# Kernel optimization log

Hardware: AMD Instinct MI355X
Metric: run time of the kernel (lower is better)

The kernel has to match this reference:

```python
import jax, jax.numpy as jnp
import numpy as np
import math

D_MODEL = 1024
NUM_HEADS = 16
D_K = D_MODEL // NUM_HEADS
SEQ = 2048
BATCH = 2


def setup_inputs() -> dict:
    key = jax.random.key(0)
    ks = jax.random.split(key, 11)
    s = 1.0 / math.sqrt(D_MODEL)
    return {
        "query": jax.random.normal(ks[0], (SEQ, BATCH, D_MODEL), jnp.float32),
        "key": jax.random.normal(ks[1], (SEQ, BATCH, D_MODEL), jnp.float32),
        "value": jax.random.normal(ks[2], (SEQ, BATCH, D_MODEL), jnp.float32),
        "Wq": jax.random.normal(ks[3], (D_MODEL, D_MODEL), jnp.float32) * s,
        "bq": jnp.zeros((D_MODEL,), jnp.float32),
        "Wk": jax.random.normal(ks[4], (D_MODEL, D_MODEL), jnp.float32) * s,
        "bk": jnp.zeros((D_MODEL,), jnp.float32),
        "Wv": jax.random.normal(ks[5], (D_MODEL, D_MODEL), jnp.float32) * s,
        "bv": jnp.zeros((D_MODEL,), jnp.float32),
        "Wo": jax.random.normal(ks[6], (D_MODEL, D_MODEL), jnp.float32) * s,
        "bo": jnp.zeros((D_MODEL,), jnp.float32),
    }


def _split_heads(x):
    # [S, B, D] -> [S, B, H, d_k]
    S, B, _ = x.shape
    return x.reshape(S, B, NUM_HEADS, D_K)


def reference(query, key, value, Wq, bq, Wk, bk, Wv, bv, Wo, bo):
    # torch Linear: y = x @ W.T + b
    q = _split_heads(query @ Wq.T + bq)   # [S,B,H,dk]
    k = _split_heads(key @ Wk.T + bk)
    v = _split_heads(value @ Wv.T + bv)
    # score[q,k,b,h] = sum_d q[q,b,h,d] k[k,b,h,d]
    score = jnp.einsum('qbhd,kbhd->qkbh', q, k) / math.sqrt(D_K)
    attn = jax.nn.softmax(score, axis=1)  # Softmax(dim=1) == over key axis
    out = jnp.einsum('qkbh,kbhd->qbhd', attn, v)  # [S,B,H,dk]
    S, B = out.shape[0], out.shape[1]
    out = out.reshape(S, B, NUM_HEADS * D_K)
    return out @ Wo.T + bo
```

## Files before the change

### kernel.cpp

```cpp
#include <hip/hip_runtime.h>

typedef unsigned short u16;
typedef short s16x8 __attribute__((ext_vector_type(8)));
typedef short s16x4 __attribute__((ext_vector_type(4)));
typedef float f32x4 __attribute__((ext_vector_type(4)));

#define MFMA_BF16(A,B,C) __builtin_amdgcn_mfma_f32_16x16x32_bf16(A,B,C,0,0,0)

#if defined(__has_builtin)
#if __has_builtin(__builtin_amdgcn_mfma_f32_16x16x16bf16_1k)
#define HAVE_MFMA16 1
#define MFMA16(A,B,C) __builtin_amdgcn_mfma_f32_16x16x16bf16_1k(A,B,C,0,0,0)
#endif
#endif

static constexpr int DMODEL = 1024;
static constexpr int SEQn   = 2048;
static constexpr int BATCH  = 2;
static constexpr int NH     = 16;
static constexpr int DKn    = 64;
static constexpr int ROWST  = BATCH*DMODEL;
static constexpr float QSCALE = 0.18033688011112042f;

__device__ __forceinline__ u16 f2bf(float f) {
    unsigned u = __builtin_bit_cast(unsigned, f);
    u += 0x7FFFu + ((u >> 16) & 1u);
    return (u16)(u >> 16);
}

#if defined(__has_builtin)
#if __has_builtin(__builtin_amdgcn_cvt_pk_bf16_f32)
#define HAVE_PKBF16 1
#endif
#endif
#ifdef HAVE_PKBF16
typedef __bf16 bf16x2 __attribute__((ext_vector_type(2)));
__device__ __forceinline__ unsigned pk2bf(float a, float b) {
    bf16x2 t = __builtin_amdgcn_cvt_pk_bf16_f32(a, b);
    return __builtin_bit_cast(unsigned, t);
}
#else
__device__ __forceinline__ unsigned pk2bf(float a, float b) {
    return (unsigned)f2bf(a) | ((unsigned)f2bf(b) << 16);
}
#endif

__device__ __forceinline__ void gld_lds16(const u16* g, u16* l) {
    __builtin_amdgcn_global_load_lds(
        (const __attribute__((address_space(1))) void*)g,
        (__attribute__((address_space(3))) void*)l,
        16, 0, 0);
}

__global__ void cvt_bf16(const float* __restrict__ q, const float* __restrict__ k,
                         const float* __restrict__ v, const float* __restrict__ wq,
                         const float* __restrict__ wk, const float* __restrict__ wv,
                         const float* __restrict__ wo,
                         u16* __restrict__ qb, u16* __restrict__ kb, u16* __restrict__ vb,
                         u16* __restrict__ wqb, u16* __restrict__ wkb, u16* __restrict__ wvb,
                         u16* __restrict__ wob)
{
    const int z = blockIdx.z;
    const float* S; u16* D; size_t n;
    switch (z) {
        case 0: S = q;  D = qb;  n = 4194304; break;
        case 1: S = k;  D = kb;  n = 4194304; break;
        case 2: S = v;  D = vb;  n = 4194304; break;
        case 3: S = wq; D = wqb; n = 1048576; break;
        case 4: S = wk; D = wkb; n = 1048576; break;
        case 5: S = wv; D = wvb; n = 1048576; break;
        default: S = wo; D = wob; n = 1048576; break;
    }
    const size_t i = ((size_t)blockIdx.x * 256 + threadIdx.x) * 8;
    if (i >= n) return;
    float4 a = *(const float4*)(S + i);
    float4 b = *(const float4*)(S + i + 4);
    uint4 pk;
    pk.x = pk2bf(a.x, a.y); pk.y = pk2bf(a.z, a.w);
    pk.z = pk2bf(b.x, b.y); pk.w = pk2bf(b.z, b.w);
    *(uint4*)(D + i) = pk;
}

__global__ __launch_bounds__(512, 2)
void gemm_qkv(const u16* __restrict__ A0, const u16* __restrict__ A1, const u16* __restrict__ A2,
              const u16* __restrict__ W0, const u16* __restrict__ W1, const u16* __restrict__ W2,
              const float* __restrict__ B0, const float* __restrict__ B1, const float* __restrict__ B2,
              void* __restrict__ O0, void* __restrict__ O1, void* __restrict__ O2)
{
    const u16* A; const u16* W; const float* bias; void* Outv;
    const int z = blockIdx.z;
    if (z == 0)      { A = A0; W = W0; bias = B0; Outv = O0; }
    else if (z == 1) { A = A1; W = W1; bias = B1; Outv = O1; }
    else             { A = A2; W = W2; bias = B2; Outv = O2; }

    __shared__ alignas(16) u16 SH[65536];

    const int tid  = threadIdx.x;
    const int wave = tid >> 6, lane = tid & 63;
    const int quad = lane >> 4, col = lane & 15;
    const int wr = wave >> 2;
    const int wn = wave & 3;
    const int m0 = blockIdx.y * 256, n0 = blockIdx.x * 256;

    f32x4 acc[8][4];
#pragma unroll
    for (int i = 0; i < 8; ++i)
#pragma unroll
        for (int j = 0; j < 4; ++j) acc[i][j] = f32x4{0.f,0.f,0.f,0.f};

    auto stageT = [&](int t) {
        const int slot = t & 3;
        const int k0 = t * 32;
        u16* Ad = SH + slot * 8192;
        u16* Bd = SH + 32768 + slot * 8192;
#pragma unroll
        for (int i = 0; i < 2; ++i) {
            const int idx = i*512 + wave*64 + lane;
            const int row = idx >> 2;
            const int s = idx & 3;
            const int g = s ^ ((row >> 1) & 3);
            gld_lds16(A + (size_t)(m0 + row)*DMODEL + k0 + g*8, Ad + (i*512 + wave*64)*8);
            gld_lds16(W + (size_t)(n0 + row)*DMODEL + k0 + g*8, Bd + (i*512 + wave*64)*8);
        }
    };

    auto compute = [&](int slot) {
        const u16* As_ = SH + slot * 8192;
        const u16* Bs_ = SH + 32768 + slot * 8192;
        s16x8 bfr[4], af[4];
#pragma unroll
        for (int fj = 0; fj < 4; ++fj) {
            const int rb = wn*64 + fj*16 + col;
            bfr[fj] = *(const s16x8*)&Bs_[rb*32 + (quad ^ ((rb >> 1) & 3))*8];
        }
#pragma unroll
        for (int fi = 0; fi < 4; ++fi) {
            const int ra = wr*128 + fi*16 + col;
            af[fi] = *(const s16x8*)&As_[ra*32 + (quad ^ ((ra >> 1) & 3))*8];
        }
        __builtin_amdgcn_s_setprio(1);
#pragma unroll
        for (int fi = 0; fi < 4; ++fi)
#pragma unroll
            for (int fj = 0; fj < 4; ++fj)
                acc[fi][fj] = MFMA_BF16(af[fi], bfr[fj], acc[fi][fj]);
        __builtin_amdgcn_s_setprio(0);
#pragma unroll
        for (int fi = 0; fi < 4; ++fi) {
            const int ra = wr*128 + (4 + fi)*16 + col;
            af[fi] = *(const s16x8*)&As_[ra*32 + (quad ^ ((ra >> 1) & 3))*8];
        }
        __builtin_amdgcn_s_setprio(1);
#pragma unroll
        for (int fi = 0; fi < 4; ++fi)
#pragma unroll
            for (int fj = 0; fj < 4; ++fj)
                acc[4 + fi][fj] = MFMA_BF16(af[fi], bfr[fj], acc[4 + fi][fj]);
        __builtin_amdgcn_s_setprio(0);
    };

    stageT(0); stageT(1); stageT(2);

    for (int t = 0; t < 30; ++t) {
        asm volatile("s_waitcnt vmcnt(8)" ::: "memory");
        __builtin_amdgcn_s_barrier();
        asm volatile("" ::: "memory");
        if (t < 29) stageT(t + 3);
        compute(t & 3);
    }
    asm volatile("s_waitcnt vmcnt(4)" ::: "memory");
    __builtin_amdgcn_s_barrier();
    asm volatile("" ::: "memory");
    compute(2);
    asm volatile("s_waitcnt vmcnt(0)" ::: "memory");
    __builtin_amdgcn_s_barrier();
    asm volatile("" ::: "memory");
    compute(3);

    float bv[4];
#pragma unroll
    for (int fj = 0; fj < 4; ++fj) bv[fj] = bias[n0 + wn*64 + fj*16 + col];

    if (z < 2) {
        u16* Out = (u16*)Outv;
        const float osc = (z == 0) ? QSCALE : 1.f;
#pragma unroll
        for (int fi = 0; fi < 8; ++fi)
#pragma unroll
            for (int fj = 0; fj < 4; ++fj) {
                const int n = n0 + wn*64 + fj*16 + col;
#pragma unroll
                for (int r = 0; r < 4; ++r) {
                    const int m = m0 + wr*128 + fi*16 + quad*4 + r;
                    Out[(size_t)m*DMODEL + n] = f2bf((acc[fi][fj][r] + bv[fj])*osc);
                }
            }
    } else {
        u16* Out = (u16*)Outv;
        u16* T = SH;
#pragma unroll
        for (int p = 0; p < 2; ++p) {
            __syncthreads();
            if (wr == p) {
#pragma unroll
                for (int fi = 0; fi < 8; ++fi)
#pragma unroll
                    for (int fj = 0; fj < 4; ++fj) {
                        const int nl = wn*64 + fj*16 + col;
#pragma unroll
                        for (int r = 0; r < 4; ++r)
                            T[(fi*16 + quad*4 + r)*257 + nl] = f2bf(acc[fi][fj][r] + bv[fj]);
                    }
            }
            __syncthreads();
            const int s0 = (m0 >> 1) + p*64;
#pragma unroll
            for (int t = 0; t < 8; ++t) {
                const int c = t*512 + tid;
                const int sc = c & 7;
                const int nl = (c >> 3) & 255;
                const int bb = c >> 11;
                u16 e[8];
#pragma unroll
                for (int j = 0; j < 8; ++j)
                    e[j] = T[((sc*8 + j)*2 + bb)*257 + nl];
                uint4 x; __builtin_memcpy(&x, e, 16);
                const int ng = n0 + nl, hh = ng >> 6, dd = ng & 63;
                *(uint4*)(Out + (((size_t)bb*NH + hh)*DKn + dd)*SEQn + s0 + sc*8) = x;
            }
        }
    }
}

template<bool FINAL>
__global__ __launch_bounds__(256, 2)
void gemm_bt(const u16* __restrict__ A0, const u16* __restrict__ A1, const u16* __restrict__ A2,
             const u16* __restrict__ W0, const u16* __restrict__ W1, const u16* __restrict__ W2,
             const float* __restrict__ B0, const float* __restrict__ B1, const float* __restrict__ B2,
             void* __restrict__ O0, void* __restrict__ O1, void* __restrict__ O2)
{
    const u16* A; const u16* W; const float* bias; void* Outv;
    const int z = blockIdx.z;
    if (z == 0)      { A = A0; W = W0; bias = B0; Outv = O0; }
    else if (z == 1) { A = A1; W = W1; bias = B1; Outv = O1; }
    else             { A = A2; W = W2; bias = B2; Outv = O2; }

    __shared__ alignas(16) u16 SH[FINAL ? 128*128 : 129*128];
    u16* As = SH;
    u16* Bs = SH + 128*64;

    const int tid  = threadIdx.x;
    const int wave = tid >> 6, lane = tid & 63;
    const int quad = lane >> 4, col = lane & 15;
    const int wm = wave & 1, wn = wave >> 1;
    const int m0 = blockIdx.y * 128, n0 = blockIdx.x * 128;

    f32x4 acc[4][4];
#pragma unroll
    for (int i = 0; i < 4; ++i)
#pragma unroll
        for (int j = 0; j < 4; ++j) acc[i][j] = f32x4{0.f,0.f,0.f,0.f};

    for (int kt = 0; kt < DMODEL/64; ++kt) {
        if (kt) __syncthreads();
        const int k0 = kt*64;
#pragma unroll
        for (int i = 0; i < 4; ++i) {
            const int chunk = (i*4 + wave)*64 + lane;
            const int row = chunk >> 3;
            const int kk = ((chunk & 7) ^ (row & 7)) * 8;
            gld_lds16(A + (size_t)(m0 + row)*DMODEL + (k0 + kk), &As[(i*4 + wave)*512]);
            gld_lds16(W + (size_t)(n0 + row)*DMODEL + (k0 + kk), &Bs[(i*4 + wave)*512]);
        }
        __syncthreads();
#pragma unroll
        for (int ks = 0; ks < 2; ++ks) {
            s16x8 af[4], bfr[4];
#pragma unroll
            for (int t = 0; t < 4; ++t) {
                const int ra = wm*64 + t*16 + col;
                af[t]  = *(const s16x8*)&As[ra*64 + (((ks*4 + quad) ^ (ra & 7))*8)];
                const int rb = wn*64 + t*16 + col;
                bfr[t] = *(const s16x8*)&Bs[rb*64 + (((ks*4 + quad) ^ (rb & 7))*8)];
            }
#pragma unroll
            for (int i = 0; i < 4; ++i)
#pragma unroll
                for (int j = 0; j < 4; ++j)
                    acc[i][j] = MFMA_BF16(af[i], bfr[j], acc[i][j]);
        }
    }

    float bv[4];
#pragma unroll
    for (int j = 0; j < 4; ++j) bv[j] = bias[n0 + wn*64 + j*16 + col];

    if (FINAL) {
#pragma unroll
        for (int i = 0; i < 4; ++i)
#pragma unroll
            for (int j = 0; j < 4; ++j) {
                const int n = n0 + wn*64 + j*16 + col;
#pragma unroll
                for (int r = 0; r < 4; ++r) {
                    const int m = m0 + wm*64 + i*16 + quad*4 + r;
                    ((float*)Outv)[(size_t)m*DMODEL + n] = acc[i][j][r] + bv[j];
                }
            }
    } else {
        const float osc = (z == 0) ? QSCALE : 1.f;
        const int SST = (z == 2) ? 129 : 128;
        __syncthreads();
#pragma unroll
        for (int i = 0; i < 4; ++i)
#pragma unroll
            for (int j = 0; j < 4; ++j) {
                const int nl = wn*64 + j*16 + col;
#pragma unroll
                for (int r = 0; r < 4; ++r) {
                    const int ml = wm*64 + i*16 + quad*4 + r;
                    SH[ml*SST + nl] = f2bf((acc[i][j][r] + bv[j])*osc);
                }
            }
        __syncthreads();
        u16* Out = (u16*)Outv;
        if (z < 2) {
#pragma unroll
            for (int t = 0; t < 8; ++t) {
                const int c = t*256 + tid;
                const int ml = c >> 4, n8 = (c & 15)*8;
                uint4 x = *(const uint4*)&SH[ml*128 + n8];
                *(uint4*)(Out + (size_t)(m0 + ml)*DMODEL + n0 + n8) = x;
            }
        } else {
            const int s0 = m0 >> 1;
#pragma unroll
            for (int t = 0; t < 8; ++t) {
                const int c = t*256 + tid;
                const int sc = c & 7;
                const int nl = (c >> 3) & 127;
                const int bb = c >> 10;
                u16 e[8];
#pragma unroll
                for (int j = 0; j < 8; ++j)
                    e[j] = SH[((sc*8 + j)*2 + bb)*129 + nl];
                uint4 x; __builtin_memcpy(&x, e, 16);
                const int ng = n0 + nl, hh = ng >> 6, dd = ng & 63;
                *(uint4*)(Out + (((size_t)bb*NH + hh)*DKn + dd)*SEQn + s0 + sc*8) = x;
            }
        }
    }
}

__global__ __launch_bounds__(256, 4)
void attn_fwd(const u16* __restrict__ Q, const u16* __restrict__ K,
              const u16* __restrict__ Vt, u16* __restrict__ O)
{
    __shared__ alignas(16) u16 Ks[128*64];
    __shared__ alignas(16) u16 Vs[64*128];

    const int qt = blockIdx.x, bh = blockIdx.y;
    const int b = bh >> 4, h = bh & 15;
    const int tid = threadIdx.x;
    const int wave = tid >> 6, lane = tid & 63;
    const int quad = lane >> 4, col = lane & 15;

    const u16* Qh = Q + b*DMODEL + h*DKn;
    const u16* Kh = K + b*DMODEL + h*DKn;
    const u16* Vh = Vt + (size_t)bh*DKn*SEQn;

    const int q0 = qt*64 + wave*16;
    s16x8 qf[2];
#pragma unroll
    for (int ks = 0; ks < 2; ++ks)
        qf[ks] = *(const s16x8*)(Qh + (size_t)(q0 + col)*ROWST + ks*32 + quad*8);

    const short ONEBF = (short)0x3F80;
    const s16x4 ones = {ONEBF, ONEBF, ONEBF, ONEBF};

    f32x4 o[4];
    f32x4 lacc = f32x4{0.f,0.f,0.f,0.f};
#pragma unroll
    for (int dt = 0; dt < 4; ++dt) o[dt] = f32x4{0.f,0.f,0.f,0.f};

    for (int kt = 0; kt < SEQn/128; ++kt) {
        __syncthreads();
#pragma unroll
        for (int i = 0; i < 4; ++i) {
            {
                const int chunk = (i*4 + wave)*64 + lane;
                const int row = chunk >> 3;
                const int kk = ((chunk & 7) ^ (row & 7))*8;
                gld_lds16(Kh + (size_t)(kt*128 + row)*ROWST + kk, &Ks[(i*4 + wave)*512]);
            }
            {
                const int chunk = (i*4 + wave)*64 + lane;
                const int d = chunk >> 4;
                const int kk = ((chunk & 15) ^ (d & 15))*8;
                gld_lds16(Vh + (size_t)d*SEQn + kt*128 + kk, &Vs[(i*4 + wave)*512]);
            }
        }
        __syncthreads();

        f32x4 sfr[8];
#pragma unroll
        for (int nt = 0; nt < 8; ++nt) sfr[nt] = f32x4{0.f,0.f,0.f,0.f};
#pragma unroll
        for (int ks = 0; ks < 2; ++ks) {
            s16x8 kf[8];
#pragma unroll
            for (int nt = 0; nt < 8; ++nt) {
                const int key = nt*16 + col;
                kf[nt] = *(const s16x8*)&Ks[key*64 + (((ks*4 + quad) ^ (key & 7))*8)];
            }
#pragma unroll
            for (int nt = 0; nt < 8; ++nt)
                sfr[nt] = MFMA_BF16(kf[nt], qf[ks], sfr[nt]);
        }

        s16x4 pk[8];
#pragma unroll
        for (int nt = 0; nt < 8; ++nt) {
            float p0 = __builtin_amdgcn_exp2f(sfr[nt][0]);
            float p1 = __builtin_amdgcn_exp2f(sfr[nt][1]);
            float p2 = __builtin_amdgcn_exp2f(sfr[nt][2]);
            float p3 = __builtin_amdgcn_exp2f(sfr[nt][3]);
            unsigned w[2] = { pk2bf(p0, p1), pk2bf(p2, p3) };
            __builtin_memcpy(&pk[nt], w, 8);
        }

#ifdef HAVE_MFMA16
#pragma unroll
        for (int c = 0; c < 8; ++c) {
            lacc = MFMA16(ones, pk[c], lacc);
#pragma unroll
            for (int dt = 0; dt < 4; ++dt) {
                const int d = dt*16 + col;
                const s16x4 vfr = *(const s16x4*)&Vs[d*128 + (((c*2 + (quad>>1)) ^ (d & 15))*8) + (quad & 1)*4];
                o[dt] = MFMA16(vfr, pk[c], o[dt]);
            }
        }
#else
        const int a0 = (32*(quad & 1) + col)*4;
        const s16x8 ones8 = {ONEBF,ONEBF,ONEBF,ONEBF,ONEBF,ONEBF,ONEBF,ONEBF};
#pragma unroll
        for (int ksp = 0; ksp < 4; ++ksp) {
            int pA[2], pB[2];
            __builtin_memcpy(pA, &pk[ksp*2], 8);
            __builtin_memcpy(pB, &pk[ksp*2 + 1], 8);
            int w[4];
#pragma unroll
            for (int hh = 0; hh < 2; ++hh) {
                const int ad = a0 + hh*64;
                const int xA0 = __builtin_amdgcn_ds_bpermute(ad, pA[0]);
                const int xA1 = __builtin_amdgcn_ds_bpermute(ad, pA[1]);
                const int xB0 = __builtin_amdgcn_ds_bpermute(ad, pB[0]);
                const int xB1 = __builtin_amdgcn_ds_bpermute(ad, pB[1]);
                w[hh*2]     = (quad >= 2) ? xB0 : xA0;
                w[hh*2 + 1] = (quad >= 2) ? xB1 : xA1;
            }
            s16x8 pfr; __builtin_memcpy(&pfr, w, 16);
            lacc = MFMA_BF16(ones8, pfr, lacc);
#pragma unroll
            for (int dt = 0; dt < 4; ++dt) {
                const int d = dt*16 + col;
                const s16x8 vfr = *(const s16x8*)&Vs[d*128 + (((ksp*4 + quad) ^ (d & 15))*8)];
                o[dt] = MFMA_BF16(vfr, pfr, o[dt]);
            }
        }
#endif
    }

    const float inv = 1.f / lacc[0];
    const int srow = q0 + col;
#pragma unroll
    for (int dt = 0; dt < 4; ++dt) {
        uint2 pko;
        pko.x = pk2bf(o[dt][0]*inv, o[dt][1]*inv);
        pko.y = pk2bf(o[dt][2]*inv, o[dt][3]*inv);
        *(uint2*)(O + ((size_t)srow*BATCH + b)*DMODEL + h*DKn + dt*16 + quad*4) = pko;
    }
}

extern "C" void kernel_launch(void* const* d_in, const int* in_sizes, int n_in,
                              void* d_out, int out_size, void* d_ws, size_t ws_size,
                              hipStream_t stream)
{
    const float* q  = (const float*)d_in[0];
    const float* k  = (const float*)d_in[1];
    const float* v  = (const float*)d_in[2];
    const float* Wq = (const float*)d_in[3];
    const float* bq = (const float*)d_in[4];
    const float* Wk = (const float*)d_in[5];
    const float* bk = (const float*)d_in[6];
    const float* Wv = (const float*)d_in[7];
    const float* bv = (const float*)d_in[8];
    const float* Wo = (const float*)d_in[9];
    const float* bo = (const float*)d_in[10];
    float* out = (float*)d_out;

    const size_t N = (size_t)SEQn * BATCH * DMODEL;
    const size_t NW = (size_t)DMODEL * DMODEL;
    u16* qb  = (u16*)d_ws;
    u16* kb  = qb + N;
    u16* vb  = kb + N;
    u16* wqb = vb + N;
    u16* wkb = wqb + NW;
    u16* wvb = wkb + NW;
    u16* wob = wvb + NW;
    u16* Qw  = wob + NW;
    u16* Kw  = Qw + N;
    u16* Vtw = Kw + N;
    u16* AO  = qb;

    cvt_bf16<<<dim3(2048, 1, 7), 256, 0, stream>>>(q, k, v, Wq, Wk, Wv, Wo,
                                                   qb, kb, vb, wqb, wkb, wvb, wob);
    gemm_qkv<<<dim3(4, 16, 3), 512, 0, stream>>>(qb, kb, vb, wqb, wkb, wvb,
                                                 bq, bk, bv, Qw, Kw, Vtw);
    attn_fwd<<<dim3(32, 32), 256, 0, stream>>>(Qw, Kw, Vtw, AO);
    gemm_bt<true><<<dim3(8, 32, 1), 256, 0, stream>>>(AO, AO, AO, wob, wob, wob,
                                                      bo, bo, bo, out, out, out);
}
```

Measured before the change: 229.5 us.

## Load K/V fragments directly from global memory with XCD-aware block mapping

The attention kernel drops its shared-memory staging of K and V tiles and the two barriers per iteration. Each wave now reads its MFMA fragments straight from global memory. Blocks are remapped on a 1-D grid so that every XCD handles four (batch, head) pairs, which keeps K/V reuse inside one L2. The softmax denominator moves from an extra MFMA against a ones vector to an fp32 running sum reduced with shuffles. The risk is that the four waves now re-read the same K/V data through cache with less coalesced accesses instead of sharing it in LDS.

```diff
diff --git a/kernel.cpp b/kernel.cpp
--- a/kernel.cpp
+++ b/kernel.cpp
@@ -356,11 +356,13 @@
 void attn_fwd(const u16* __restrict__ Q, const u16* __restrict__ K,
               const u16* __restrict__ Vt, u16* __restrict__ O)
 {
-    __shared__ alignas(16) u16 Ks[128*64];
-    __shared__ alignas(16) u16 Vs[64*128];
-
-    const int qt = blockIdx.x, bh = blockIdx.y;
+    const int bid = blockIdx.x;
+    const int xcd = bid & 7;
+    const int jj  = bid >> 3;
+    const int bh  = xcd*4 + (jj >> 5);
+    const int qt  = jj & 31;
     const int b = bh >> 4, h = bh & 15;
+
     const int tid = threadIdx.x;
     const int wave = tid >> 6, lane = tid & 63;
     const int quad = lane >> 4, col = lane & 15;
@@ -375,32 +377,14 @@
     for (int ks = 0; ks < 2; ++ks)
         qf[ks] = *(const s16x8*)(Qh + (size_t)(q0 + col)*ROWST + ks*32 + quad*8);
 
-    const short ONEBF = (short)0x3F80;
-    const s16x4 ones = {ONEBF, ONEBF, ONEBF, ONEBF};
-
     f32x4 o[4];
-    f32x4 lacc = f32x4{0.f,0.f,0.f,0.f};
+    float dsum = 0.f;
 #pragma unroll
     for (int dt = 0; dt < 4; ++dt) o[dt] = f32x4{0.f,0.f,0.f,0.f};
 
     for (int kt = 0; kt < SEQn/128; ++kt) {
-        __syncthreads();
-#pragma unroll
-        for (int i = 0; i < 4; ++i) {
-            {
-                const int chunk = (i*4 + wave)*64 + lane;
-                const int row = chunk >> 3;
-                const int kk = ((chunk & 7) ^ (row & 7))*8;
-                gld_lds16(Kh + (size_t)(kt*128 + row)*ROWST + kk, &Ks[(i*4 + wave)*512]);
-            }
-            {
-                const int chunk = (i*4 + wave)*64 + lane;
-                const int d = chunk >> 4;
-                const int kk = ((chunk & 15) ^ (d & 15))*8;
-                gld_lds16(Vh + (size_t)d*SEQn + kt*128 + kk, &Vs[(i*4 + wave)*512]);
-            }
-        }
-        __syncthreads();
+        const u16* Kt = Kh + (size_t)(kt*128)*ROWST;
+        const u16* Vkt = Vh + kt*128;
 
         f32x4 sfr[8];
 #pragma unroll
@@ -409,10 +393,8 @@
         for (int ks = 0; ks < 2; ++ks) {
             s16x8 kf[8];
 #pragma unroll
-            for (int nt = 0; nt < 8; ++nt) {
-                const int key = nt*16 + col;
-                kf[nt] = *(const s16x8*)&Ks[key*64 + (((ks*4 + quad) ^ (key & 7))*8)];
-            }
+            for (int nt = 0; nt < 8; ++nt)
+                kf[nt] = *(const s16x8*)(Kt + (size_t)(nt*16 + col)*ROWST + ks*32 + quad*8);
 #pragma unroll
             for (int nt = 0; nt < 8; ++nt)
                 sfr[nt] = MFMA_BF16(kf[nt], qf[ks], sfr[nt]);
@@ -425,6 +407,7 @@
             float p1 = __builtin_amdgcn_exp2f(sfr[nt][1]);
             float p2 = __builtin_amdgcn_exp2f(sfr[nt][2]);
             float p3 = __builtin_amdgcn_exp2f(sfr[nt][3]);
+            dsum += (p0 + p1) + (p2 + p3);
             unsigned w[2] = { pk2bf(p0, p1), pk2bf(p2, p3) };
             __builtin_memcpy(&pk[nt], w, 8);
         }
@@ -432,17 +415,15 @@
 #ifdef HAVE_MFMA16
 #pragma unroll
         for (int c = 0; c < 8; ++c) {
-            lacc = MFMA16(ones, pk[c], lacc);
 #pragma unroll
             for (int dt = 0; dt < 4; ++dt) {
-                const int d = dt*16 + col;
-                const s16x4 vfr = *(const s16x4*)&Vs[d*128 + (((c*2 + (quad>>1)) ^ (d & 15))*8) + (quad & 1)*4];
+                const s16x4 vfr = *(const s16x4*)(Vkt + (size_t)(dt*16 + col)*SEQn
+                                                  + c*16 + (quad>>1)*8 + (quad&1)*4);
                 o[dt] = MFMA16(vfr, pk[c], o[dt]);
             }
         }
 #else
         const int a0 = (32*(quad & 1) + col)*4;
-        const s16x8 ones8 = {ONEBF,ONEBF,ONEBF,ONEBF,ONEBF,ONEBF,ONEBF,ONEBF};
 #pragma unroll
         for (int ksp = 0; ksp < 4; ++ksp) {
             int pA[2], pB[2];
@@ -460,18 +441,21 @@
                 w[hh*2 + 1] = (quad >= 2) ? xB1 : xA1;
             }
             s16x8 pfr; __builtin_memcpy(&pfr, w, 16);
-            lacc = MFMA_BF16(ones8, pfr, lacc);
 #pragma unroll
             for (int dt = 0; dt < 4; ++dt) {
-                const int d = dt*16 + col;
-                const s16x8 vfr = *(const s16x8*)&Vs[d*128 + (((ksp*4 + quad) ^ (d & 15))*8)];
+                const s16x8 vfr = *(const s16x8*)(Vkt + (size_t)(dt*16 + col)*SEQn
+                                                  + (ksp*4 + quad)*8);
                 o[dt] = MFMA_BF16(vfr, pfr, o[dt]);
             }
         }
 #endif
     }
 
-    const float inv = 1.f / lacc[0];
+    float den = dsum;
+    den += __shfl_xor(den, 16, 64);
+    den += __shfl_xor(den, 32, 64);
+    const float inv = 1.f / den;
+
     const int srow = q0 + col;
 #pragma unroll
     for (int dt = 0; dt < 4; ++dt) {
@@ -517,7 +501,7 @@
                                                    qb, kb, vb, wqb, wkb, wvb, wob);
     gemm_qkv<<<dim3(4, 16, 3), 512, 0, stream>>>(qb, kb, vb, wqb, wkb, wvb,
                                                  bq, bk, bv, Qw, Kw, Vtw);
-    attn_fwd<<<dim3(32, 32), 256, 0, stream>>>(Qw, Kw, Vtw, AO);
+    attn_fwd<<<dim3(1024), 256, 0, stream>>>(Qw, Kw, Vtw, AO);
     gemm_bt<true><<<dim3(8, 32, 1), 256, 0, stream>>>(AO, AO, AO, wob, wob, wob,
                                                       bo, bo, bo, out, out, out);
 }
```

Result: slower. 503.0 us (+119.1%).
